# Optimization experiments

Measured on AMD Instinct MI355X. Metric: run time of the kernel, lower is better.

Reference implementation:

```python
import jax, jax.numpy as jnp
from jax import lax
import numpy as np

BS, T, C, N, K, D, H = 8, 32, 64, 4096, 32, 64, 64
NB, BSZ, NG, BPG = 4, 8, 1, 4  # dendritic tree: 4 branches of 8, 1 group of 4 branches


def setup_inputs() -> dict:
    key = jax.random.key(0)
    ks = jax.random.split(key, 16)
    fc1_scale = (2.0 / (5 * D + H)) ** 0.5
    return {
        "cc_signals": jax.random.normal(ks[0], (BS, T, C, D), jnp.float32),
        "h": jax.random.normal(ks[1], (BS, N, D), jnp.float32) * 0.1,
        "prev_messages": jnp.tanh(jax.random.normal(ks[2], (BS, N, D), jnp.float32)),
        "trace_prim": jax.random.normal(ks[3], (BS, N, D), jnp.float32) * 0.1,
        "trace_key": jax.random.normal(ks[4], (BS, N, D), jnp.float32) * 0.1,
        "primitives": jax.random.normal(ks[5], (N, D), jnp.float32),
        "key_p": jax.random.normal(ks[6], (N, D), jnp.float32),
        "decay_logit": jax.random.normal(ks[7], (N,), jnp.float32) * 0.1,
        "dendrite_branch_w": 1.0 / BSZ + jax.random.normal(ks[8], (N, NB, BSZ, D), jnp.float32) * 0.05,
        "dendrite_group_w": 1.0 / BPG + jax.random.normal(ks[9], (N, NG, BPG, D), jnp.float32) * 0.05,
        "fc1_w": jax.random.normal(ks[10], (N, 5 * D, H), jnp.float32) * fc1_scale,
        "fc1_b": jnp.zeros((N, H), jnp.float32),
        "fc2_w": jax.random.normal(ks[11], (N, H, 3), jnp.float32) * 0.05,
        "fc2_b": jnp.zeros((N, 3), jnp.float32),
        "mod_lr_logit": jnp.full((1,), -2.0, jnp.float32),
        "conn_indices": jax.random.randint(ks[12], (N, K), 0, N),
        "stride": 4,
    }


def reference(cc_signals, h, prev_messages, trace_prim, trace_key, primitives,
              key_p, decay_logit, dendrite_branch_w, dendrite_group_w,
              fc1_w, fc1_b, fc2_w, fc2_b, mod_lr_logit, conn_indices, stride):
    bsz, tseg, c, d = cc_signals.shape
    n = primitives.shape[0]
    k = conn_indices.shape[1]
    nb, bsize = dendrite_branch_w.shape[1], dendrite_branch_w.shape[2]
    ng, bpg = dendrite_group_w.shape[1], dendrite_group_w.shape[2]
    n_tree = ng * bpg * bsize

    # --- per-neuron modulator MLP (once per segment) ---
    prim_b = jnp.broadcast_to(primitives[None], (bsz, n, d))
    key_b = jnp.broadcast_to(key_p[None], (bsz, n, d))
    mod_input = jnp.concatenate([h, trace_prim, trace_key, prim_b, key_b], axis=-1)  # [B,N,5D]
    x = jnp.tanh(jnp.einsum('bnd,ndh->bnh', mod_input, fc1_w) + fc1_b)
    out = jnp.einsum('bnh,nho->bno', x, fc2_w) + fc2_b  # [B,N,3]
    gate_prim = jnp.tanh(out[..., 0:1])
    gate_key = jnp.tanh(out[..., 1:2])
    decay_mod = out[..., 2]

    mod_lr = jax.nn.sigmoid(mod_lr_logit[0])
    tp_dir = trace_prim / jnp.maximum(jnp.linalg.norm(trace_prim, axis=-1, keepdims=True), 1e-8)
    tk_dir = trace_key / jnp.maximum(jnp.linalg.norm(trace_key, axis=-1, keepdims=True), 1e-8)
    eff_prim = primitives[None] + mod_lr * gate_prim * tp_dir        # [B,N,D]
    eff_key = key_p[None] + mod_lr * gate_key * tk_dir               # [B,N,D]
    eff_decay = jax.nn.sigmoid(decay_logit[None] + decay_mod)[..., None]  # [B,N,1]

    def dendritic(weighted):  # weighted: [B,N,K,D]
        tree = weighted[:, :, :n_tree].reshape(bsz, n, nb, bsize, d)
        branch = jnp.tanh(jnp.sum(tree * dendrite_branch_w[None], axis=3))   # [B,N,nb,D]
        grouped = branch.reshape(bsz, n, ng, bpg, d)
        group = jnp.tanh(jnp.sum(grouped * dendrite_group_w[None], axis=3))  # [B,N,ng,D]
        received = group.mean(axis=2)
        if n_tree < k:  # static
            leftover = weighted[:, :, n_tree:].sum(axis=2)
            frac = n_tree / k
            received = frac * received + (1.0 - frac) * leftover
        return received

    def update(hh, pm, cc_t):
        nb_msgs = pm[:, conn_indices]                                # gather: [B,N,K,D]
        sim = jnp.einsum('bnd,bnkd->bnk', eff_key, nb_msgs)
        weighted = jax.nn.sigmoid(sim)[..., None] * nb_msgs
        received = dendritic(weighted)
        received = received.at[:, :c].add(cc_t)
        h2 = eff_decay * hh + (1.0 - eff_decay) * received
        return h2, jnp.tanh(h2 * eff_prim)

    def step(carry, inp):
        hh, pm = carry
        t, cc_t = inp
        hh, pm = lax.cond(t % stride == 0,
                          lambda a, b: update(a, b, cc_t),
                          lambda a, b: (a, b), hh, pm)
        return (hh, pm), pm[:, :c]

    ts = jnp.arange(tseg)
    cc_tfirst = jnp.transpose(cc_signals, (1, 0, 2, 3))  # [T,B,C,D]
    _, outs = lax.scan(step, (h, prev_messages), (ts, cc_tfirst))
    return jnp.transpose(outs, (1, 0, 2, 3))  # [B,T,C,D]
```

## Files before the change

### kernel.cpp

```cpp
#include <hip/hip_runtime.h>
#include <hip/hip_bf16.h>

#define BS 8
#define T_ 32
#define C_ 64
#define N_ 4096
#define K_ 32
#define D_ 64
#define H_ 64

typedef __hip_bfloat16 bf16;

__device__ __forceinline__ float fexp2(float x){ return __builtin_amdgcn_exp2f(x); }
__device__ __forceinline__ float frcp(float x){ return __builtin_amdgcn_rcpf(x); }
__device__ __forceinline__ float sigm(float x){ return frcp(1.f + fexp2(-1.44269504f*x)); }
__device__ __forceinline__ float tanh_(float x){ return 1.f - 2.f*frcp(1.f + fexp2(2.88539008f*x)); }

__device__ __forceinline__ float ld1(const bf16* p, int i){ return __bfloat162float(p[i]); }
__device__ __forceinline__ float ld1(const float* p, int i){ return p[i]; }
__device__ __forceinline__ void st1(bf16* p, int i, float v){ p[i] = __float2bfloat16(v); }
__device__ __forceinline__ void st1(float* p, int i, float v){ p[i] = v; }

__device__ __forceinline__ float allsum(float v){
  #pragma unroll
  for (int d = 1; d < 64; d <<= 1) v += __shfl_xor(v, d, 64);
  return v;
}

__device__ __forceinline__ bool is_bf16(const void* mll){
  return ((const unsigned short*)mll)[0] == 0xC000u;
}

template<typename TI>
__device__ __forceinline__ void mod_body(
    const TI* h_in, const TI* tp, const TI* tk, const TI* prim, const TI* keyp,
    const TI* dlog, const TI* w1, const TI* b1, const TI* w2, const TI* bb2, const TI* mll,
    float* cp_a, float* ck_a, float* dc_a, float* sin_f, int n, int lane)
{
  #pragma unroll
  for (int b = 0; b < BS; b++){
    int src = (b*N_ + n)*D_ + lane;
    sin_f[b*320       + lane] = ld1(h_in, src);
    sin_f[b*320 + 64  + lane] = ld1(tp, src);
    sin_f[b*320 + 128 + lane] = ld1(tk, src);
    sin_f[b*320 + 192 + lane] = ld1(prim, n*D_ + lane);
    sin_f[b*320 + 256 + lane] = ld1(keyp, n*D_ + lane);
  }
  __syncthreads();
  float acc[BS] = {};
  const TI* wrow = w1 + n*(320*H_) + lane;
  #pragma unroll 4
  for (int d = 0; d < 320; d++){
    float wv = ld1(wrow, d*H_);
    #pragma unroll
    for (int b = 0; b < BS; b++)
      acc[b] = fmaf(sin_f[b*320 + d], wv, acc[b]);
  }
  float bb  = ld1(b1, n*H_ + lane);
  float w20 = ld1(w2, n*(H_*3) + lane*3 + 0);
  float w21 = ld1(w2, n*(H_*3) + lane*3 + 1);
  float w22 = ld1(w2, n*(H_*3) + lane*3 + 2);
  float bo0 = ld1(bb2, n*3 + 0);
  float bo1 = ld1(bb2, n*3 + 1);
  float bo2 = ld1(bb2, n*3 + 2);
  float mlr = sigm(ld1(mll, 0));
  float dl  = ld1(dlog, n);
  #pragma unroll
  for (int b = 0; b < BS; b++){
    float x  = tanh_(acc[b] + bb);
    float o0 = allsum(x*w20) + bo0;
    float o1 = allsum(x*w21) + bo1;
    float o2 = allsum(x*w22) + bo2;
    float tpd = sin_f[b*320 + 64  + lane];
    float tkd = sin_f[b*320 + 128 + lane];
    float npn = fmaxf(sqrtf(allsum(tpd*tpd)), 1e-8f);
    float nkn = fmaxf(sqrtf(allsum(tkd*tkd)), 1e-8f);
    if (lane == 0){
      int g = b*N_ + n;
      cp_a[g] = mlr * tanh_(o0) * frcp(npn);
      ck_a[g] = mlr * tanh_(o1) * frcp(nkn);
      dc_a[g] = sigm(dl + o2);
    }
  }
}

__global__ __launch_bounds__(64) void k_mod(
    const void* h_in, const void* tp, const void* tk, const void* prim, const void* keyp,
    const void* dlog, const void* w1, const void* b1, const void* w2, const void* bb2,
    const void* mll, float* cp_a, float* ck_a, float* dc_a)
{
  __shared__ float sin_f[BS*320];
  int n = blockIdx.x, lane = threadIdx.x;
  if (is_bf16(mll))
    mod_body<bf16>((const bf16*)h_in,(const bf16*)tp,(const bf16*)tk,(const bf16*)prim,
                   (const bf16*)keyp,(const bf16*)dlog,(const bf16*)w1,(const bf16*)b1,
                   (const bf16*)w2,(const bf16*)bb2,(const bf16*)mll,
                   cp_a, ck_a, dc_a, sin_f, n, lane);
  else
    mod_body<float>((const float*)h_in,(const float*)tp,(const float*)tk,(const float*)prim,
                    (const float*)keyp,(const float*)dlog,(const float*)w1,(const float*)b1,
                    (const float*)w2,(const float*)bb2,(const float*)mll,
                    cp_a, ck_a, dc_a, sin_f, n, lane);
}

template<typename TH>
__global__ __launch_bounds__(256) void k_inith(const void* h_in, const void* mll, TH* h_ws){
  int i = blockIdx.x*256 + threadIdx.x;
  if (is_bf16(mll)) st1(h_ws, i, ld1((const bf16*)h_in, i));
  else              st1(h_ws, i, ld1((const float*)h_in, i));
}

template<typename TS>
__global__ __launch_bounds__(256) void k_initpm(const void* pm_in, const void* mll, TS* pm_ws){
  int i = blockIdx.x*256 + threadIdx.x;
  if (is_bf16(mll)) st1(pm_ws, i, ld1((const bf16*)pm_in, i));
  else              st1(pm_ws, i, ld1((const float*)pm_in, i));
}

template<typename TI, typename TS, typename TH>
__device__ __forceinline__ void step_body(
    const TS* pm_in, TS* pm_out, TH* h_ws,
    const float* cp_a, const float* ck_a, const float* dc_a,
    const TI* tp, const TI* tk, const TI* prim, const TI* keyp,
    const TI* dbw, const TI* dgw, const TI* cc, const int* conn,
    TI* out, int tcur)
{
  int lane = threadIdx.x & 63;
  int n = blockIdx.x*4 + (threadIdx.x >> 6);
  int b = blockIdx.y;
  int g = b*N_ + n;
  int rb = g*D_ + lane;
  float keyd = fmaf(ck_a[g], ld1(tk, rb), ld1(keyp, n*D_ + lane));
  int idxv = conn[n*K_ + (lane & 31)];
  const TS* pmb = pm_in + (size_t)(b*N_)*D_ + lane;
  const TI* bwb = dbw + n*(K_*D_) + lane;

  float msg[K_];
  #pragma unroll
  for (int k = 0; k < K_; k++){
    int m = __builtin_amdgcn_readlane(idxv, k);
    msg[k] = ld1(pmb, m*D_);
  }

  float r[16];
  {
    bool hb = (lane & 1) != 0;
    #pragma unroll
    for (int j = 0; j < 16; j++){
      float a  = keyd * msg[2*j];
      float bq = keyd * msg[2*j+1];
      float lo = hb ? bq : a;
      float hi = hb ? a  : bq;
      r[j] = lo + __shfl_xor(hi, 1, 64);
    }
  }
  #pragma unroll
  for (int s = 1; s < 5; s++){
    int m = 1 << s;
    bool hb = (lane & m) != 0;
    #pragma unroll
    for (int j = 0; j < (16 >> s); j++){
      float a  = r[2*j];
      float bq = r[2*j+1];
      float lo = hb ? bq : a;
      float hi = hb ? a  : bq;
      r[j] = lo + __shfl_xor(hi, m, 64);
    }
  }
  float simv = r[0] + __shfl_xor(r[0], 32, 64);
  float wv = sigm(simv);

  float accb[4] = {};
  #pragma unroll
  for (int k = 0; k < K_; k++){
    float w = __uint_as_float(__builtin_amdgcn_readlane(__float_as_uint(wv), k));
    accb[k>>3] = fmaf(w*msg[k], ld1(bwb, k*D_), accb[k>>3]);
  }

  const TI* gwb = dgw + n*(4*D_) + lane;
  float gg = 0.f;
  #pragma unroll
  for (int j = 0; j < 4; j++)
    gg = fmaf(tanh_(accb[j]), ld1(gwb, j*D_), gg);
  float recv = tanh_(gg);
  if (n < C_) recv += ld1(cc, ((b*T_ + tcur)*C_ + n)*D_ + lane);
  float dec = dc_a[g];
  float hv = ld1(h_ws, rb);
  float h2 = recv + dec*(hv - recv);
  st1(h_ws, rb, h2);
  float effp = fmaf(cp_a[g], ld1(tp, rb), ld1(prim, n*D_ + lane));
  float pmv = tanh_(h2 * effp);
  st1(pm_out, rb, pmv);
  if (n < C_){
    #pragma unroll
    for (int dt = 0; dt < 4; dt++)
      st1(out, ((b*T_ + tcur + dt)*C_ + n)*D_ + lane, pmv);
  }
}

template<typename TS, typename TH>
__global__ __launch_bounds__(256) void k_step(
    const TS* pm_in, TS* pm_out, TH* h_ws,
    const float* cp_a, const float* ck_a, const float* dc_a,
    const void* tp, const void* tk, const void* prim, const void* keyp,
    const void* dbw, const void* dgw, const void* cc, const int* conn,
    void* out, const void* mll, int tcur)
{
  if (is_bf16(mll))
    step_body<bf16,TS,TH>(pm_in, pm_out, h_ws, cp_a, ck_a, dc_a,
        (const bf16*)tp,(const bf16*)tk,(const bf16*)prim,(const bf16*)keyp,
        (const bf16*)dbw,(const bf16*)dgw,(const bf16*)cc, conn, (bf16*)out, tcur);
  else
    step_body<float,TS,TH>(pm_in, pm_out, h_ws, cp_a, ck_a, dc_a,
        (const float*)tp,(const float*)tk,(const float*)prim,(const float*)keyp,
        (const float*)dbw,(const float*)dgw,(const float*)cc, conn, (float*)out, tcur);
}

template<typename TS, typename TH>
static void launch_all(void* const* d_in, void* d_out, void* d_ws, hipStream_t stream)
{
  const void* cc   = d_in[0];
  const void* h_in = d_in[1];
  const void* pmsg = d_in[2];
  const void* tp   = d_in[3];
  const void* tk   = d_in[4];
  const void* prim = d_in[5];
  const void* keyp = d_in[6];
  const void* dlog = d_in[7];
  const void* dbw  = d_in[8];
  const void* dgw  = d_in[9];
  const void* w1   = d_in[10];
  const void* b1   = d_in[11];
  const void* w2   = d_in[12];
  const void* bb2  = d_in[13];
  const void* mll  = d_in[14];
  const int* conn  = (const int*)d_in[15];

  const int NE = BS*N_*D_;
  const int BSN = BS*N_;
  char* p = (char*)d_ws;
  TH* h_ws = (TH*)p;            p += (size_t)NE*sizeof(TH);
  float* cp_a = (float*)p;      p += (size_t)BSN*4;
  float* ck_a = (float*)p;      p += (size_t)BSN*4;
  float* dc_a = (float*)p;      p += (size_t)BSN*4;
  TS* pm0 = (TS*)p;             p += (size_t)NE*sizeof(TS);
  TS* pm1 = (TS*)p;

  k_inith<TH><<<NE/256, 256, 0, stream>>>(h_in, mll, h_ws);
  k_initpm<TS><<<NE/256, 256, 0, stream>>>(pmsg, mll, pm0);
  k_mod<<<N_, 64, 0, stream>>>(h_in, tp, tk, prim, keyp, dlog, w1, b1, w2, bb2, mll,
                               cp_a, ck_a, dc_a);
  for (int s = 0; s < 8; s++){
    const TS* pin = (s & 1) ? pm1 : pm0;
    TS* pout = (s & 1) ? pm0 : pm1;
    k_step<TS,TH><<<dim3(N_/4, BS), 256, 0, stream>>>(
        pin, pout, h_ws, cp_a, ck_a, dc_a,
        tp, tk, prim, keyp, dbw, dgw, cc, conn, d_out, mll, 4*s);
  }
}

extern "C" void kernel_launch(void* const* d_in, const int* in_sizes, int n_in,
                              void* d_out, int out_size, void* d_ws, size_t ws_size,
                              hipStream_t stream)
{
  (void)in_sizes; (void)n_in; (void)out_size;
  const size_t NE = (size_t)BS*N_*D_;
  const size_t gates = 3ull*BS*N_*4;
  if (ws_size >= NE*4 + gates + 2*NE*4)
    launch_all<float, float>(d_in, d_out, d_ws, stream);
  else if (ws_size >= NE*4 + gates + 2*NE*2)
    launch_all<bf16, float>(d_in, d_out, d_ws, stream);
  else
    launch_all<bf16, bf16>(d_in, d_out, d_ws, stream);
}
```

Baseline: 1.016 ms.

## Reuse per-neuron weights across batch in step kernel; register-broadcast MLP inputs

The step kernel now handles all 8 batch elements inside one block per neuron group. It loads the dendrite branch/group weights, key and primitive once into registers and reuses them across the batch, instead of reloading them for each batch via a batch grid dimension. The modulator kernel drops its shared-memory input staging and broadcasts the per-dimension inputs with readlane. It also computes the batch-invariant primitive/key contribution once and shares it across the batch. The trade-off is an 8x smaller grid with a serial batch loop, which lowers parallelism and occupancy, plus higher register pressure.

```diff
diff --git a/kernel.cpp b/kernel.cpp
--- a/kernel.cpp
+++ b/kernel.cpp
@@ -21,6 +21,10 @@
 __device__ __forceinline__ void st1(bf16* p, int i, float v){ p[i] = __float2bfloat16(v); }
 __device__ __forceinline__ void st1(float* p, int i, float v){ p[i] = v; }
 
+__device__ __forceinline__ float rl(float x, int j){
+  return __uint_as_float(__builtin_amdgcn_readlane(__float_as_uint(x), j));
+}
+
 __device__ __forceinline__ float allsum(float v){
   #pragma unroll
   for (int d = 1; d < 64; d <<= 1) v += __shfl_xor(v, d, 64);
@@ -35,27 +39,39 @@
 __device__ __forceinline__ void mod_body(
     const TI* h_in, const TI* tp, const TI* tk, const TI* prim, const TI* keyp,
     const TI* dlog, const TI* w1, const TI* b1, const TI* w2, const TI* bb2, const TI* mll,
-    float* cp_a, float* ck_a, float* dc_a, float* sin_f, int n, int lane)
-{
+    float* cp_a, float* ck_a, float* dc_a, int n, int lane)
+{
+  float h_r[BS], tp_r[BS], tk_r[BS];
   #pragma unroll
   for (int b = 0; b < BS; b++){
     int src = (b*N_ + n)*D_ + lane;
-    sin_f[b*320       + lane] = ld1(h_in, src);
-    sin_f[b*320 + 64  + lane] = ld1(tp, src);
-    sin_f[b*320 + 128 + lane] = ld1(tk, src);
-    sin_f[b*320 + 192 + lane] = ld1(prim, n*D_ + lane);
-    sin_f[b*320 + 256 + lane] = ld1(keyp, n*D_ + lane);
-  }
-  __syncthreads();
+    h_r[b]  = ld1(h_in, src);
+    tp_r[b] = ld1(tp, src);
+    tk_r[b] = ld1(tk, src);
+  }
+  float prim_r = ld1(prim, n*D_ + lane);
+  float keyp_r = ld1(keyp, n*D_ + lane);
+
+  const TI* wrow = w1 + n*(320*H_) + lane;
   float acc[BS] = {};
-  const TI* wrow = w1 + n*(320*H_) + lane;
+  float accs = 0.f;
   #pragma unroll 4
-  for (int d = 0; d < 320; d++){
-    float wv = ld1(wrow, d*H_);
-    #pragma unroll
-    for (int b = 0; b < BS; b++)
-      acc[b] = fmaf(sin_f[b*320 + d], wv, acc[b]);
-  }
+  for (int j = 0; j < 64; j++){
+    float w0v = ld1(wrow, (      j)*H_);
+    float w1v = ld1(wrow, ( 64 + j)*H_);
+    float w2v = ld1(wrow, (128 + j)*H_);
+    float w3v = ld1(wrow, (192 + j)*H_);
+    float w4v = ld1(wrow, (256 + j)*H_);
+    #pragma unroll
+    for (int b = 0; b < BS; b++){
+      acc[b] = fmaf(rl(h_r[b],  j), w0v, acc[b]);
+      acc[b] = fmaf(rl(tp_r[b], j), w1v, acc[b]);
+      acc[b] = fmaf(rl(tk_r[b], j), w2v, acc[b]);
+    }
+    accs = fmaf(rl(prim_r, j), w3v, accs);
+    accs = fmaf(rl(keyp_r, j), w4v, accs);
+  }
+
   float bb  = ld1(b1, n*H_ + lane);
   float w20 = ld1(w2, n*(H_*3) + lane*3 + 0);
   float w21 = ld1(w2, n*(H_*3) + lane*3 + 1);
@@ -67,12 +83,12 @@
   float dl  = ld1(dlog, n);
   #pragma unroll
   for (int b = 0; b < BS; b++){
-    float x  = tanh_(acc[b] + bb);
+    float x  = tanh_(acc[b] + accs + bb);
     float o0 = allsum(x*w20) + bo0;
     float o1 = allsum(x*w21) + bo1;
     float o2 = allsum(x*w22) + bo2;
-    float tpd = sin_f[b*320 + 64  + lane];
-    float tkd = sin_f[b*320 + 128 + lane];
+    float tpd = tp_r[b];
+    float tkd = tk_r[b];
     float npn = fmaxf(sqrtf(allsum(tpd*tpd)), 1e-8f);
     float nkn = fmaxf(sqrtf(allsum(tkd*tkd)), 1e-8f);
     if (lane == 0){
@@ -89,18 +105,17 @@
     const void* dlog, const void* w1, const void* b1, const void* w2, const void* bb2,
     const void* mll, float* cp_a, float* ck_a, float* dc_a)
 {
-  __shared__ float sin_f[BS*320];
   int n = blockIdx.x, lane = threadIdx.x;
   if (is_bf16(mll))
     mod_body<bf16>((const bf16*)h_in,(const bf16*)tp,(const bf16*)tk,(const bf16*)prim,
                    (const bf16*)keyp,(const bf16*)dlog,(const bf16*)w1,(const bf16*)b1,
                    (const bf16*)w2,(const bf16*)bb2,(const bf16*)mll,
-                   cp_a, ck_a, dc_a, sin_f, n, lane);
+                   cp_a, ck_a, dc_a, n, lane);
   else
     mod_body<float>((const float*)h_in,(const float*)tp,(const float*)tk,(const float*)prim,
                     (const float*)keyp,(const float*)dlog,(const float*)w1,(const float*)b1,
                     (const float*)w2,(const float*)bb2,(const float*)mll,
-                    cp_a, ck_a, dc_a, sin_f, n, lane);
+                    cp_a, ck_a, dc_a, n, lane);
 }
 
 template<typename TH>
@@ -126,75 +141,85 @@
     TI* out, int tcur)
 {
   int lane = threadIdx.x & 63;
-  int n = blockIdx.x*4 + (threadIdx.x >> 6);
-  int b = blockIdx.y;
-  int g = b*N_ + n;
-  int rb = g*D_ + lane;
-  float keyd = fmaf(ck_a[g], ld1(tk, rb), ld1(keyp, n*D_ + lane));
+  int n    = blockIdx.x*4 + (threadIdx.x >> 6);
+
   int idxv = conn[n*K_ + (lane & 31)];
-  const TS* pmb = pm_in + (size_t)(b*N_)*D_ + lane;
-  const TI* bwb = dbw + n*(K_*D_) + lane;
-
-  float msg[K_];
-  #pragma unroll
-  for (int k = 0; k < K_; k++){
-    int m = __builtin_amdgcn_readlane(idxv, k);
-    msg[k] = ld1(pmb, m*D_);
-  }
-
-  float r[16];
-  {
-    bool hb = (lane & 1) != 0;
-    #pragma unroll
-    for (int j = 0; j < 16; j++){
-      float a  = keyd * msg[2*j];
-      float bq = keyd * msg[2*j+1];
-      float lo = hb ? bq : a;
-      float hi = hb ? a  : bq;
-      r[j] = lo + __shfl_xor(hi, 1, 64);
-    }
-  }
-  #pragma unroll
-  for (int s = 1; s < 5; s++){
-    int m = 1 << s;
-    bool hb = (lane & m) != 0;
-    #pragma unroll
-    for (int j = 0; j < (16 >> s); j++){
-      float a  = r[2*j];
-      float bq = r[2*j+1];
-      float lo = hb ? bq : a;
-      float hi = hb ? a  : bq;
-      r[j] = lo + __shfl_xor(hi, m, 64);
-    }
-  }
-  float simv = r[0] + __shfl_xor(r[0], 32, 64);
-  float wv = sigm(simv);
-
-  float accb[4] = {};
-  #pragma unroll
-  for (int k = 0; k < K_; k++){
-    float w = __uint_as_float(__builtin_amdgcn_readlane(__float_as_uint(wv), k));
-    accb[k>>3] = fmaf(w*msg[k], ld1(bwb, k*D_), accb[k>>3]);
-  }
-
-  const TI* gwb = dgw + n*(4*D_) + lane;
-  float gg = 0.f;
-  #pragma unroll
-  for (int j = 0; j < 4; j++)
-    gg = fmaf(tanh_(accb[j]), ld1(gwb, j*D_), gg);
-  float recv = tanh_(gg);
-  if (n < C_) recv += ld1(cc, ((b*T_ + tcur)*C_ + n)*D_ + lane);
-  float dec = dc_a[g];
-  float hv = ld1(h_ws, rb);
-  float h2 = recv + dec*(hv - recv);
-  st1(h_ws, rb, h2);
-  float effp = fmaf(cp_a[g], ld1(tp, rb), ld1(prim, n*D_ + lane));
-  float pmv = tanh_(h2 * effp);
-  st1(pm_out, rb, pmv);
-  if (n < C_){
-    #pragma unroll
-    for (int dt = 0; dt < 4; dt++)
-      st1(out, ((b*T_ + tcur + dt)*C_ + n)*D_ + lane, pmv);
+  float bw_r[K_];
+  #pragma unroll
+  for (int k = 0; k < K_; k++) bw_r[k] = ld1(dbw, n*(K_*D_) + k*D_ + lane);
+  float gw_r[4];
+  #pragma unroll
+  for (int j = 0; j < 4; j++) gw_r[j] = ld1(dgw, n*(4*D_) + j*D_ + lane);
+  float keyp_r = ld1(keyp, n*D_ + lane);
+  float prim_r = ld1(prim, n*D_ + lane);
+
+  #pragma unroll 1
+  for (int b = 0; b < BS; b++){
+    int g  = b*N_ + n;
+    int rb = g*D_ + lane;
+    float keyd = fmaf(ck_a[g], ld1(tk, rb), keyp_r);
+    const TS* pmb = pm_in + (size_t)(b*N_)*D_ + lane;
+
+    float msg[K_];
+    #pragma unroll
+    for (int k = 0; k < K_; k++){
+      int m = __builtin_amdgcn_readlane(idxv, k);
+      msg[k] = ld1(pmb, m*D_);
+    }
+
+    float r[16];
+    {
+      bool hb = (lane & 1) != 0;
+      #pragma unroll
+      for (int j = 0; j < 16; j++){
+        float a  = keyd * msg[2*j];
+        float bq = keyd * msg[2*j+1];
+        float lo = hb ? bq : a;
+        float hi = hb ? a  : bq;
+        r[j] = lo + __shfl_xor(hi, 1, 64);
+      }
+    }
+    #pragma unroll
+    for (int s = 1; s < 5; s++){
+      int m = 1 << s;
+      bool hb = (lane & m) != 0;
+      #pragma unroll
+      for (int j = 0; j < (16 >> s); j++){
+        float a  = r[2*j];
+        float bq = r[2*j+1];
+        float lo = hb ? bq : a;
+        float hi = hb ? a  : bq;
+        r[j] = lo + __shfl_xor(hi, m, 64);
+      }
+    }
+    float simv = r[0] + __shfl_xor(r[0], 32, 64);
+    float wv = sigm(simv);
+
+    float accb[4] = {};
+    #pragma unroll
+    for (int k = 0; k < K_; k++){
+      float w = rl(wv, k);
+      accb[k>>3] = fmaf(w*msg[k], bw_r[k], accb[k>>3]);
+    }
+
+    float gg = 0.f;
+    #pragma unroll
+    for (int j = 0; j < 4; j++)
+      gg = fmaf(tanh_(accb[j]), gw_r[j], gg);
+    float recv = tanh_(gg);
+    if (n < C_) recv += ld1(cc, ((b*T_ + tcur)*C_ + n)*D_ + lane);
+    float dec = dc_a[g];
+    float hv = ld1(h_ws, rb);
+    float h2 = recv + dec*(hv - recv);
+    st1(h_ws, rb, h2);
+    float effp = fmaf(cp_a[g], ld1(tp, rb), prim_r);
+    float pmv = tanh_(h2 * effp);
+    st1(pm_out, rb, pmv);
+    if (n < C_){
+      #pragma unroll
+      for (int dt = 0; dt < 4; dt++)
+        st1(out, ((b*T_ + tcur + dt)*C_ + n)*D_ + lane, pmv);
+    }
   }
 }
 
@@ -253,7 +278,7 @@
   for (int s = 0; s < 8; s++){
     const TS* pin = (s & 1) ? pm1 : pm0;
     TS* pout = (s & 1) ? pm0 : pm1;
-    k_step<TS,TH><<<dim3(N_/4, BS), 256, 0, stream>>>(
+    k_step<TS,TH><<<dim3(N_/4), 256, 0, stream>>>(
         pin, pout, h_ws, cp_a, ck_a, dc_a,
         tp, tk, prim, keyp, dbw, dgw, cc, conn, d_out, mll, 4*s);
   }
```

Result: faster. 917.0 us (-9.7%).
